# Kernel optimization log

Measured on AMD Instinct MI355X. Metric: run time of the kernel, lower is better.

## Reference

```python
import jax, jax.numpy as jnp
import numpy as np

N_NODES = 200000
N_EDGES = 600000
NUM_GRAPHS = 20000
IN_DIM = 128
HID = 128
HEADS1 = 4
OUT1 = HID // HEADS1  # 32
NEG_SLOPE = 0.2
LN_EPS = 1e-5


def setup_inputs() -> dict:
    key = jax.random.key(0)
    ks = jax.random.split(key, 12)
    x = jax.random.normal(ks[0], (N_NODES, IN_DIM), dtype=jnp.float32)
    edge_index = jax.random.randint(ks[1], (2, N_EDGES), 0, N_NODES, dtype=jnp.int64)
    batch = jnp.sort(jax.random.randint(ks[2], (N_NODES,), 0, NUM_GRAPHS, dtype=jnp.int64))
    s1 = 1.0 / np.sqrt(IN_DIM)
    s2 = 1.0 / np.sqrt(HID)
    W1 = jax.random.normal(ks[3], (IN_DIM, HEADS1 * OUT1), dtype=jnp.float32) * s1
    att_src1 = jax.random.normal(ks[4], (HEADS1, OUT1), dtype=jnp.float32) * s1
    att_dst1 = jax.random.normal(ks[5], (HEADS1, OUT1), dtype=jnp.float32) * s1
    b1 = jnp.zeros((HEADS1 * OUT1,), dtype=jnp.float32)
    W2 = jax.random.normal(ks[6], (HID, HID), dtype=jnp.float32) * s2
    att_src2 = jax.random.normal(ks[7], (1, HID), dtype=jnp.float32) * s2
    att_dst2 = jax.random.normal(ks[8], (1, HID), dtype=jnp.float32) * s2
    b2 = jnp.zeros((HID,), dtype=jnp.float32)
    ln_gamma = jnp.ones((HID,), dtype=jnp.float32)
    ln_beta = jnp.zeros((HID,), dtype=jnp.float32)
    return dict(x=x, edge_index=edge_index, batch=batch,
                W1=W1, att_src1=att_src1, att_dst1=att_dst1, b1=b1,
                W2=W2, att_src2=att_src2, att_dst2=att_dst2, b2=b2,
                ln_gamma=ln_gamma, ln_beta=ln_beta)


def gat_conv(x, W, att_src, att_dst, bias, edge_index, heads, out_ch):
    # PyG GATConv (concat=True, add_self_loops=True, eval mode / no dropout)
    n = x.shape[0]
    loop = jnp.arange(n, dtype=edge_index.dtype)
    src = jnp.concatenate([edge_index[0], loop])
    dst = jnp.concatenate([edge_index[1], loop])
    h = (x @ W).reshape(n, heads, out_ch)          # [N,H,C]
    a_src = jnp.einsum('nhc,hc->nh', h, att_src)    # [N,H]
    a_dst = jnp.einsum('nhc,hc->nh', h, att_dst)
    alpha = a_src[src] + a_dst[dst]                 # [E,H]
    alpha = jax.nn.leaky_relu(alpha, NEG_SLOPE)
    # segment softmax over incoming edges of each dst node
    m = jax.lax.stop_gradient(jax.ops.segment_max(alpha, dst, num_segments=n))
    e = jnp.exp(alpha - m[dst])
    denom = jax.ops.segment_sum(e, dst, num_segments=n)
    coef = e / denom[dst]                           # [E,H]
    msg = h[src] * coef[:, :, None]                 # [E,H,C]
    out = jax.ops.segment_sum(msg, dst, num_segments=n)  # [N,H,C]
    return out.reshape(n, heads * out_ch) + bias


def layer_norm(x, gamma, beta):
    mu = jnp.mean(x, axis=-1, keepdims=True)
    var = jnp.mean(jnp.square(x - mu), axis=-1, keepdims=True)
    return (x - mu) * jax.lax.rsqrt(var + LN_EPS) * gamma + beta


def reference(x, edge_index, batch, W1, att_src1, att_dst1, b1,
              W2, att_src2, att_dst2, b2, ln_gamma, ln_beta):
    h1 = jax.nn.relu(gat_conv(x, W1, att_src1, att_dst1, b1, edge_index, HEADS1, OUT1))
    h2 = gat_conv(h1, W2, att_src2, att_dst2, b2, edge_index, 1, HID)
    h2 = layer_norm(h2, ln_gamma, ln_beta)
    # global mean pool per graph
    sums = jax.ops.segment_sum(h2, batch, num_segments=NUM_GRAPHS)   # [G,HID]
    cnts = jax.ops.segment_sum(jnp.ones((h2.shape[0],), h2.dtype), batch, num_segments=NUM_GRAPHS)
    return sums / jnp.maximum(cnts, 1.0)[:, None]
```

## Files before the change

### kernel.cpp

```cpp
#include <hip/hip_runtime.h>
#include <cstdint>
#include <cstddef>

#define N_NODES_C 200000
#define N_EDGES_C 600000
#define NUM_GRAPHS_C 20000

constexpr float NEG_SLOPE = 0.2f;
constexpr float LN_EPS = 1e-5f;

typedef __attribute__((ext_vector_type(8))) short bf16x8;
typedef __attribute__((ext_vector_type(4))) float f32x4;

static __device__ __forceinline__ unsigned short f2bf(float f) {
  unsigned u = __float_as_uint(f);
  u = (u + 0x7fffu + ((u >> 16) & 1u)) >> 16;
  return (unsigned short)u;
}
static __device__ __forceinline__ float bf2f(unsigned short s) {
  return __uint_as_float(((unsigned)s) << 16);
}


__global__ __launch_bounds__(256) void count_deg_kernel(const int* __restrict__ dst,
                                                        int* __restrict__ deg, int E) {
  int e = blockIdx.x * 256 + threadIdx.x;
  if (e < E) atomicAdd(&deg[dst[e]], 1);
}

__global__ __launch_bounds__(256) void scan_kernel(const int* __restrict__ in,
                                                   int* __restrict__ out,
                                                   int* __restrict__ bsums, int n) {
  __shared__ int ss[256];
  int t = threadIdx.x;
  int base = blockIdx.x * 1024 + t * 4;
  int v[4];
  int s = 0;
#pragma unroll
  for (int j = 0; j < 4; ++j) {
    v[j] = (base + j < n) ? in[base + j] : 0;
    s += v[j];
  }
  ss[t] = s;
  __syncthreads();
  for (int off = 1; off < 256; off <<= 1) {
    int x = (t >= off) ? ss[t - off] : 0;
    __syncthreads();
    ss[t] += x;
    __syncthreads();
  }
  int incl = ss[t];
  int excl = incl - s;
  if (bsums != nullptr && t == 255) bsums[blockIdx.x] = incl;
  int run = excl;
#pragma unroll
  for (int j = 0; j < 4; ++j) {
    if (base + j < n) out[base + j] = run;
    run += v[j];
  }
}

__global__ __launch_bounds__(256) void scan_addoff_kernel(int* __restrict__ data,
                                                          const int* __restrict__ boff,
                                                          int n, int total) {
  int base = blockIdx.x * 1024 + threadIdx.x * 4;
  int add = boff[blockIdx.x];
#pragma unroll
  for (int j = 0; j < 4; ++j) {
    if (base + j < n) data[base + j] += add;
  }
  if (blockIdx.x == 0 && threadIdx.x == 0) data[n] = total;
}

__global__ __launch_bounds__(256) void fill_csr_kernel(const int* __restrict__ src,
                                                       const int* __restrict__ dst,
                                                       const int* __restrict__ row_ptr,
                                                       int* __restrict__ cursor,
                                                       int* __restrict__ col, int E) {
  int e = blockIdx.x * 256 + threadIdx.x;
  if (e < E) {
    int d = dst[e];
    int p = atomicAdd(&cursor[d], 1);
    col[row_ptr[d] + p] = src[e];
  }
}


__global__ __launch_bounds__(256) void graph_ptr_kernel(const int* __restrict__ batch,
                                                        int* __restrict__ gp, int n,
                                                        int G) {
  int i = blockIdx.x * 256 + threadIdx.x;
  if (i < n) {
    int prev = (i == 0) ? -1 : batch[i - 1];
    int cur = batch[i];
#pragma unroll 1
    for (int g = prev + 1; g <= cur; ++g) gp[g] = i;
  } else if (i == n) {
    int last = batch[n - 1];
#pragma unroll 1
    for (int g = last + 1; g <= G; ++g) gp[g] = n;
  }
}


__global__ __launch_bounds__(256) void wprep_kernel(const float* __restrict__ W,
                                                    unsigned short* __restrict__ Wtp) {
  int idx = blockIdx.x * 256 + threadIdx.x;
  if (idx >= 128 * 136) return;
  int n = idx / 136, k = idx % 136;
  Wtp[idx] = (k < 128) ? f2bf(W[(size_t)k * 128 + n]) : (unsigned short)0;
}


template <int H, bool A_BF16>
__global__ __launch_bounds__(256) void gemm_att_mfma(
    const void* __restrict__ Av, const unsigned short* __restrict__ Wtp,
    const float* __restrict__ att_src, const float* __restrict__ att_dst,
    unsigned short* __restrict__ Cbf, float* __restrict__ asrc,
    float* __restrict__ adst) {
  __shared__ __align__(16) unsigned short Alds[64 * 136];
  __shared__ __align__(16) unsigned short Wlds[128 * 136];
  int tid = threadIdx.x;
  int lane = tid & 63;
  int wave = tid >> 6;
  int row0 = blockIdx.x * 64;

#pragma unroll
  for (int i = 0; i < 9; ++i) {
    int ch = tid + i * 256;
    if (ch < 2176) *(bf16x8*)&Wlds[ch * 8] = *(const bf16x8*)&Wtp[(size_t)ch * 8];
  }
#pragma unroll
  for (int i = 0; i < 4; ++i) {
    int ch = tid + i * 256;
    int r = ch >> 4, c = ch & 15;
    if constexpr (A_BF16) {
      bf16x8 v = *(const bf16x8*)((const unsigned short*)Av +
                                  (size_t)(row0 + r) * 128 + c * 8);
      *(bf16x8*)&Alds[r * 136 + c * 8] = v;
    } else {
      const float* A = (const float*)Av;
      float4 v0 = *(const float4*)(A + (size_t)(row0 + r) * 128 + c * 8);
      float4 v1 = *(const float4*)(A + (size_t)(row0 + r) * 128 + c * 8 + 4);
      unsigned short tmp[8] = {f2bf(v0.x), f2bf(v0.y), f2bf(v0.z), f2bf(v0.w),
                               f2bf(v1.x), f2bf(v1.y), f2bf(v1.z), f2bf(v1.w)};
      *(bf16x8*)&Alds[r * 136 + c * 8] = *(bf16x8*)tmp;
    }
  }
  __syncthreads();

  int l15 = lane & 15;
  int lg = lane >> 4;
  int wr = wave * 16;

  f32x4 acc[8];
#pragma unroll
  for (int nt = 0; nt < 8; ++nt) acc[nt] = (f32x4){0.f, 0.f, 0.f, 0.f};

#pragma unroll
  for (int ks = 0; ks < 4; ++ks) {
    bf16x8 af = *(const bf16x8*)&Alds[(wr + l15) * 136 + ks * 32 + lg * 8];
#pragma unroll
    for (int nt = 0; nt < 8; ++nt) {
      bf16x8 bfr = *(const bf16x8*)&Wlds[(nt * 16 + l15) * 136 + ks * 32 + lg * 8];
      acc[nt] = __builtin_amdgcn_mfma_f32_16x16x32_bf16(af, bfr, acc[nt], 0, 0, 0);
    }
  }

  float vsv[8], vdv[8];
#pragma unroll
  for (int nt = 0; nt < 8; ++nt) {
    vsv[nt] = att_src[nt * 16 + l15];
    vdv[nt] = att_dst[nt * 16 + l15];
  }

#pragma unroll
  for (int r = 0; r < 4; ++r) {
    int row = row0 + wr + lg * 4 + r;
#pragma unroll
    for (int nt = 0; nt < 8; ++nt) {
      Cbf[(size_t)row * 128 + nt * 16 + l15] = f2bf(acc[nt][r]);
    }
    if constexpr (H == 4) {
      float ps[4], pd[4];
#pragma unroll
      for (int hd = 0; hd < 4; ++hd) {
        ps[hd] = acc[2 * hd][r] * vsv[2 * hd] + acc[2 * hd + 1][r] * vsv[2 * hd + 1];
        pd[hd] = acc[2 * hd][r] * vdv[2 * hd] + acc[2 * hd + 1][r] * vdv[2 * hd + 1];
#pragma unroll
        for (int off = 1; off < 16; off <<= 1) {
          ps[hd] += __shfl_xor(ps[hd], off, 64);
          pd[hd] += __shfl_xor(pd[hd], off, 64);
        }
      }
      if (l15 < 4) {
        float pss = (l15 == 0) ? ps[0] : (l15 == 1) ? ps[1] : (l15 == 2) ? ps[2] : ps[3];
        float pds = (l15 == 0) ? pd[0] : (l15 == 1) ? pd[1] : (l15 == 2) ? pd[2] : pd[3];
        asrc[(size_t)row * 4 + l15] = pss;
        adst[(size_t)row * 4 + l15] = pds;
      }
    } else {
      float ps = 0.f, pd = 0.f;
#pragma unroll
      for (int nt = 0; nt < 8; ++nt) {
        ps = fmaf(acc[nt][r], vsv[nt], ps);
        pd = fmaf(acc[nt][r], vdv[nt], pd);
      }
#pragma unroll
      for (int off = 1; off < 16; off <<= 1) {
        ps += __shfl_xor(ps, off, 64);
        pd += __shfl_xor(pd, off, 64);
      }
      if (l15 == 0) {
        asrc[row] = ps;
        adst[row] = pd;
      }
    }
  }
}


template <int H, bool RELU, bool LNOUT>
__global__ __launch_bounds__(256) void gat_agg3_kernel(
    const unsigned short* __restrict__ h, const float* __restrict__ asrc,
    const float* __restrict__ adst, const int* __restrict__ row_ptr,
    const int* __restrict__ col, const float* __restrict__ bias,
    const float* __restrict__ gamma, const float* __restrict__ beta,
    unsigned short* __restrict__ outbf, int n) {
  int wid = (blockIdx.x * 256 + threadIdx.x) >> 6;
  int lane = threadIdx.x & 63;
  int nodeA = wid * 2;
  int nodeB = nodeA + 1;
  if (nodeA >= n) return;
  bool hasB = nodeB < n;

  int e0A = row_ptr[nodeA];
  int e1A = row_ptr[nodeA + 1];
  int e1B = hasB ? row_ptr[nodeB + 1] : e1A;
  int e0B = e1A;
  int nedA = e1A - e0A;
  int nedB = e1B - e0B;

  int c0 = lane * 2;
  const int hd = (H == 1) ? 0 : (lane >> 4);

  float adA = (H == 4) ? adst[(size_t)nodeA * 4 + hd] : adst[nodeA];
  float asA = (H == 4) ? asrc[(size_t)nodeA * 4 + hd] : asrc[nodeA];
  int nB = hasB ? nodeB : nodeA;
  float adB = (H == 4) ? adst[(size_t)nB * 4 + hd] : adst[nB];
  float asB = (H == 4) ? asrc[(size_t)nB * 4 + hd] : asrc[nB];

  float xA = asA + adA; xA = (xA > 0.f) ? xA : NEG_SLOPE * xA;
  float selfeA = __expf(xA);
  float xB = asB + adB; xB = (xB > 0.f) ? xB : NEG_SLOPE * xB;
  float selfeB = __expf(xB);

  float denA = selfeA;
  float denB = selfeB;

  float2 accA, accB;
  {
    unsigned ha = *(const unsigned*)(h + (size_t)nodeA * 128 + c0);
    unsigned hb = *(const unsigned*)(h + (size_t)nB * 128 + c0);
    accA.x = bf2f((unsigned short)(ha & 0xffffu)) * selfeA;
    accA.y = bf2f((unsigned short)(ha >> 16)) * selfeA;
    accB.x = bf2f((unsigned short)(hb & 0xffffu)) * selfeB;
    accB.y = bf2f((unsigned short)(hb >> 16)) * selfeB;
  }

  int tmax = (nedA > nedB) ? nedA : nedB;
#pragma unroll 1
  for (int t = 0; t < tmax; t += 4) {
    int sA4[4], sB4[4];
    bool vA4[4], vB4[4];
#pragma unroll
    for (int i = 0; i < 4; ++i) {
      int e = t + i;
      vA4[i] = e < nedA;
      vB4[i] = hasB && e < nedB;
      sA4[i] = vA4[i] ? col[e0A + e] : nodeA;
      sB4[i] = vB4[i] ? col[e0B + e] : nodeA;
    }
    float aA4[4], aB4[4];
    unsigned hA4[4], hB4[4];
#pragma unroll
    for (int i = 0; i < 4; ++i) {
      aA4[i] = (H == 4) ? asrc[(size_t)sA4[i] * 4 + hd] : asrc[sA4[i]];
      aB4[i] = (H == 4) ? asrc[(size_t)sB4[i] * 4 + hd] : asrc[sB4[i]];
      hA4[i] = *(const unsigned*)(h + (size_t)sA4[i] * 128 + c0);
      hB4[i] = *(const unsigned*)(h + (size_t)sB4[i] * 128 + c0);
    }
#pragma unroll
    for (int i = 0; i < 4; ++i) {
      float ya = aA4[i] + adA; ya = (ya > 0.f) ? ya : NEG_SLOPE * ya;
      float eeA = vA4[i] ? __expf(ya) : 0.f;
      float yb = aB4[i] + adB; yb = (yb > 0.f) ? yb : NEG_SLOPE * yb;
      float eeB = vB4[i] ? __expf(yb) : 0.f;
      denA += eeA;
      denB += eeB;
      accA.x = fmaf(bf2f((unsigned short)(hA4[i] & 0xffffu)), eeA, accA.x);
      accA.y = fmaf(bf2f((unsigned short)(hA4[i] >> 16)), eeA, accA.y);
      accB.x = fmaf(bf2f((unsigned short)(hB4[i] & 0xffffu)), eeB, accB.x);
      accB.y = fmaf(bf2f((unsigned short)(hB4[i] >> 16)), eeB, accB.y);
    }
  }

  float invA = 1.f / denA;
  float invB = 1.f / denB;

  float bx = bias[c0], by = bias[c0 + 1];
  accA.x = fmaf(accA.x, invA, bx);
  accA.y = fmaf(accA.y, invA, by);
  accB.x = fmaf(accB.x, invB, bx);
  accB.y = fmaf(accB.y, invB, by);
  if (RELU) {
    accA.x = fmaxf(accA.x, 0.f); accA.y = fmaxf(accA.y, 0.f);
    accB.x = fmaxf(accB.x, 0.f); accB.y = fmaxf(accB.y, 0.f);
  }

  if (!LNOUT) {
    unsigned pa = (unsigned)f2bf(accA.x) | ((unsigned)f2bf(accA.y) << 16);
    *(unsigned*)(outbf + (size_t)nodeA * 128 + c0) = pa;
    if (hasB) {
      unsigned pb = (unsigned)f2bf(accB.x) | ((unsigned)f2bf(accB.y) << 16);
      *(unsigned*)(outbf + (size_t)nodeB * 128 + c0) = pb;
    }
  } else {
    float sA = accA.x + accA.y;
    float sB = accB.x + accB.y;
#pragma unroll
    for (int off = 1; off < 64; off <<= 1) {
      sA += __shfl_xor(sA, off, 64);
      sB += __shfl_xor(sB, off, 64);
    }
    float muA = sA * (1.f / 128.f), muB = sB * (1.f / 128.f);
    float dxA = accA.x - muA, dyA = accA.y - muA;
    float dxB = accB.x - muB, dyB = accB.y - muB;
    float vA = dxA * dxA + dyA * dyA;
    float vB = dxB * dxB + dyB * dyB;
#pragma unroll
    for (int off = 1; off < 64; off <<= 1) {
      vA += __shfl_xor(vA, off, 64);
      vB += __shfl_xor(vB, off, 64);
    }
    float ivA = rsqrtf(vA * (1.f / 128.f) + LN_EPS);
    float ivB = rsqrtf(vB * (1.f / 128.f) + LN_EPS);
    float gx = gamma[c0], gy = gamma[c0 + 1];
    float ex = beta[c0], ey = beta[c0 + 1];
    float oxA = fmaf(dxA * ivA, gx, ex), oyA = fmaf(dyA * ivA, gy, ey);
    unsigned pa = (unsigned)f2bf(oxA) | ((unsigned)f2bf(oyA) << 16);
    *(unsigned*)(outbf + (size_t)nodeA * 128 + c0) = pa;
    if (hasB) {
      float oxB = fmaf(dxB * ivB, gx, ex), oyB = fmaf(dyB * ivB, gy, ey);
      unsigned pb = (unsigned)f2bf(oxB) | ((unsigned)f2bf(oyB) << 16);
      *(unsigned*)(outbf + (size_t)nodeB * 128 + c0) = pb;
    }
  }
}


__global__ __launch_bounds__(256) void pool_kernel(const unsigned short* __restrict__ hln,
                                                   const int* __restrict__ gp,
                                                   float* __restrict__ out, int G) {
  int g = (blockIdx.x * 256 + threadIdx.x) >> 6;
  int lane = threadIdx.x & 63;
  if (g >= G) return;
  int s = gp[g], e = gp[g + 1];
  float ax = 0.f, ay = 0.f;
#pragma unroll 1
  for (int i = s; i < e; ++i) {
    unsigned v = *(const unsigned*)(hln + (size_t)i * 128 + lane * 2);
    ax += bf2f((unsigned short)(v & 0xffffu));
    ay += bf2f((unsigned short)(v >> 16));
  }
  int c = e - s;
  float sc = 1.f / (float)((c > 0) ? c : 1);
  *(float2*)(out + (size_t)g * 128 + lane * 2) = make_float2(ax * sc, ay * sc);
}


extern "C" void kernel_launch(void* const* d_in, const int* in_sizes, int n_in,
                              void* d_out, int out_size, void* d_ws, size_t ws_size,
                              hipStream_t stream) {
  const float* x = (const float*)d_in[0];
  const int* ei = (const int*)d_in[1];
  const int* batch = (const int*)d_in[2];
  const float* W1 = (const float*)d_in[3];
  const float* att_src1 = (const float*)d_in[4];
  const float* att_dst1 = (const float*)d_in[5];
  const float* b1 = (const float*)d_in[6];
  const float* W2 = (const float*)d_in[7];
  const float* att_src2 = (const float*)d_in[8];
  const float* att_dst2 = (const float*)d_in[9];
  const float* b2 = (const float*)d_in[10];
  const float* gamma = (const float*)d_in[11];
  const float* beta = (const float*)d_in[12];
  float* out = (float*)d_out;

  const int N = N_NODES_C, E = N_EDGES_C, G = NUM_GRAPHS_C;
  const int* src = ei;
  const int* dst = ei + E;

  float* p = (float*)d_ws;
  float* asrc1 = p; p += (size_t)N * 4;
  float* adst1 = p; p += (size_t)N * 4;
  float* asrc2 = p; p += N;
  float* adst2 = p; p += N;
  int* ip = (int*)p;
  int* deg = ip;       ip += N;
  int* cursor = ip;    ip += N;
  int* col = ip;       ip += E;
  int* bsums = ip;     ip += 256;
  int* bsums2 = ip;    ip += 256;
  int* row_ptr = ip;   ip += N + 2;
  int* graph_ptr = ip; ip += G + 2;
  unsigned short* h1bf = (unsigned short*)ip;
  unsigned short* hbbf = h1bf + (size_t)N * 128;
  unsigned short* h2bf = hbbf + (size_t)N * 128;
  unsigned short* wt1 = h2bf + (size_t)N * 128;
  unsigned short* wt2 = wt1 + 128 * 136;
  (void)ws_size; (void)in_sizes; (void)n_in; (void)out_size;

  hipMemsetAsync(deg, 0, sizeof(int) * (size_t)N, stream);
  hipMemsetAsync(cursor, 0, sizeof(int) * (size_t)N, stream);

  count_deg_kernel<<<(E + 255) / 256, 256, 0, stream>>>(dst, deg, E);
  int nblk = (N + 1023) / 1024;
  scan_kernel<<<nblk, 256, 0, stream>>>(deg, row_ptr, bsums, N);
  scan_kernel<<<1, 256, 0, stream>>>(bsums, bsums2, nullptr, nblk);
  scan_addoff_kernel<<<nblk, 256, 0, stream>>>(row_ptr, bsums2, N, E);
  fill_csr_kernel<<<(E + 255) / 256, 256, 0, stream>>>(src, dst, row_ptr, cursor, col, E);
  graph_ptr_kernel<<<(N + 1 + 255) / 256, 256, 0, stream>>>(batch, graph_ptr, N, G);
  wprep_kernel<<<(128 * 136 + 255) / 256, 256, 0, stream>>>(W1, wt1);
  wprep_kernel<<<(128 * 136 + 255) / 256, 256, 0, stream>>>(W2, wt2);

  int pairs = (N + 1) / 2;
  int pblocks = (int)(((size_t)pairs * 64 + 255) / 256);
  int gblocks = N / 64;

  gemm_att_mfma<4, false><<<gblocks, 256, 0, stream>>>(
      x, wt1, att_src1, att_dst1, h1bf, asrc1, adst1);
  gat_agg3_kernel<4, true, false><<<pblocks, 256, 0, stream>>>(
      h1bf, asrc1, adst1, row_ptr, col, b1, nullptr, nullptr, hbbf, N);

  gemm_att_mfma<1, true><<<gblocks, 256, 0, stream>>>(
      hbbf, wt2, att_src2, att_dst2, h2bf, asrc2, adst2);
  gat_agg3_kernel<1, false, true><<<pblocks, 256, 0, stream>>>(
      h2bf, asrc2, adst2, row_ptr, col, b2, gamma, beta, h1bf, N);

  pool_kernel<<<(int)(((size_t)G * 64 + 255) / 256), 256, 0, stream>>>(
      h1bf, graph_ptr, out, G);
}
```

Baseline: 297.3 us.

## Precompute per-edge attention exponentials in CSR order before aggregation

Adds an edge_score kernel that computes leaky-ReLU and exp of the attention logits per edge and scatters them into a head-major array indexed by CSR slot, recorded during CSR fill. The aggregation kernels then read these precomputed weights contiguously instead of gathering asrc for each source and evaluating exp per lane. The intent is to take the dependent random asrc gather off the aggregation critical path. The cost is two extra kernel launches, an extra edge-slot array, a scattered write pass, and reads of the column and weight arrays past the row end (masked, but EP padding is only 8).

Result: slower. 343.2 us (+15.4%).

```diff
diff --git a/kernel.cpp b/kernel.cpp
--- a/kernel.cpp
+++ b/kernel.cpp
@@ -76,12 +76,15 @@
                                                        const int* __restrict__ dst,
                                                        const int* __restrict__ row_ptr,
                                                        int* __restrict__ cursor,
-                                                       int* __restrict__ col, int E) {
+                                                       int* __restrict__ col,
+                                                       int* __restrict__ eslot, int E) {
   int e = blockIdx.x * 256 + threadIdx.x;
   if (e < E) {
     int d = dst[e];
     int p = atomicAdd(&cursor[d], 1);
-    col[row_ptr[d] + p] = src[e];
+    int slot = row_ptr[d] + p;
+    col[slot] = src[e];
+    eslot[e] = slot;
   }
 }
 
@@ -220,13 +223,39 @@
 }
 
 
+template <int H>
+__global__ __launch_bounds__(256) void edge_score_kernel(
+    const int* __restrict__ src, const int* __restrict__ dst,
+    const int* __restrict__ eslot, const float* __restrict__ asrc,
+    const float* __restrict__ adst, float* __restrict__ evt, int E, int EP) {
+  int e = blockIdx.x * 256 + threadIdx.x;
+  if (e >= E) return;
+  int s = src[e], d = dst[e], slot = eslot[e];
+  if constexpr (H == 4) {
+    float4 a = *(const float4*)(asrc + (size_t)s * 4);
+    float4 b = *(const float4*)(adst + (size_t)d * 4);
+    float v[4] = {a.x + b.x, a.y + b.y, a.z + b.z, a.w + b.w};
+#pragma unroll
+    for (int k = 0; k < 4; ++k) {
+      float x = v[k];
+      x = (x > 0.f) ? x : NEG_SLOPE * x;
+      evt[(size_t)k * EP + slot] = __expf(x);
+    }
+  } else {
+    float x = asrc[s] + adst[d];
+    x = (x > 0.f) ? x : NEG_SLOPE * x;
+    evt[slot] = __expf(x);
+  }
+}
+
+
 template <int H, bool RELU, bool LNOUT>
-__global__ __launch_bounds__(256) void gat_agg3_kernel(
+__global__ __launch_bounds__(256) void gat_agg4_kernel(
     const unsigned short* __restrict__ h, const float* __restrict__ asrc,
-    const float* __restrict__ adst, const int* __restrict__ row_ptr,
-    const int* __restrict__ col, const float* __restrict__ bias,
-    const float* __restrict__ gamma, const float* __restrict__ beta,
-    unsigned short* __restrict__ outbf, int n) {
+    const float* __restrict__ adst, const float* __restrict__ evt, int EP,
+    const int* __restrict__ row_ptr, const int* __restrict__ col,
+    const float* __restrict__ bias, const float* __restrict__ gamma,
+    const float* __restrict__ beta, unsigned short* __restrict__ outbf, int n) {
   int wid = (blockIdx.x * 256 + threadIdx.x) >> 6;
   int lane = threadIdx.x & 63;
   int nodeA = wid * 2;
@@ -243,6 +272,7 @@
 
   int c0 = lane * 2;
   const int hd = (H == 1) ? 0 : (lane >> 4);
+  const float* evh = evt + (size_t)hd * EP;
 
   float adA = (H == 4) ? adst[(size_t)nodeA * 4 + hd] : adst[nodeA];
   float asA = (H == 4) ? asrc[(size_t)nodeA * 4 + hd] : asrc[nodeA];
@@ -272,36 +302,35 @@
 #pragma unroll 1
   for (int t = 0; t < tmax; t += 4) {
     int sA4[4], sB4[4];
-    bool vA4[4], vB4[4];
+    float eA4[4], eB4[4];
 #pragma unroll
     for (int i = 0; i < 4; ++i) {
       int e = t + i;
-      vA4[i] = e < nedA;
-      vB4[i] = hasB && e < nedB;
-      sA4[i] = vA4[i] ? col[e0A + e] : nodeA;
-      sB4[i] = vB4[i] ? col[e0B + e] : nodeA;
-    }
-    float aA4[4], aB4[4];
+      bool vA = e < nedA;
+      bool vB = hasB && e < nedB;
+      int cA = col[e0A + e];
+      int cB = col[e0B + e];
+      float fA = evh[e0A + e];
+      float fB = evh[e0B + e];
+      sA4[i] = vA ? cA : nodeA;
+      sB4[i] = vB ? cB : nodeA;
+      eA4[i] = vA ? fA : 0.f;
+      eB4[i] = vB ? fB : 0.f;
+    }
     unsigned hA4[4], hB4[4];
 #pragma unroll
     for (int i = 0; i < 4; ++i) {
-      aA4[i] = (H == 4) ? asrc[(size_t)sA4[i] * 4 + hd] : asrc[sA4[i]];
-      aB4[i] = (H == 4) ? asrc[(size_t)sB4[i] * 4 + hd] : asrc[sB4[i]];
       hA4[i] = *(const unsigned*)(h + (size_t)sA4[i] * 128 + c0);
       hB4[i] = *(const unsigned*)(h + (size_t)sB4[i] * 128 + c0);
     }
 #pragma unroll
     for (int i = 0; i < 4; ++i) {
-      float ya = aA4[i] + adA; ya = (ya > 0.f) ? ya : NEG_SLOPE * ya;
-      float eeA = vA4[i] ? __expf(ya) : 0.f;
-      float yb = aB4[i] + adB; yb = (yb > 0.f) ? yb : NEG_SLOPE * yb;
-      float eeB = vB4[i] ? __expf(yb) : 0.f;
-      denA += eeA;
-      denB += eeB;
-      accA.x = fmaf(bf2f((unsigned short)(hA4[i] & 0xffffu)), eeA, accA.x);
-      accA.y = fmaf(bf2f((unsigned short)(hA4[i] >> 16)), eeA, accA.y);
-      accB.x = fmaf(bf2f((unsigned short)(hB4[i] & 0xffffu)), eeB, accB.x);
-      accB.y = fmaf(bf2f((unsigned short)(hB4[i] >> 16)), eeB, accB.y);
+      denA += eA4[i];
+      denB += eB4[i];
+      accA.x = fmaf(bf2f((unsigned short)(hA4[i] & 0xffffu)), eA4[i], accA.x);
+      accA.y = fmaf(bf2f((unsigned short)(hA4[i] >> 16)), eA4[i], accA.y);
+      accB.x = fmaf(bf2f((unsigned short)(hB4[i] & 0xffffu)), eB4[i], accB.x);
+      accB.y = fmaf(bf2f((unsigned short)(hB4[i] >> 16)), eB4[i], accB.y);
     }
   }
 
@@ -398,6 +427,7 @@
   float* out = (float*)d_out;
 
   const int N = N_NODES_C, E = N_EDGES_C, G = NUM_GRAPHS_C;
+  const int EP = E + 8;
   const int* src = ei;
   const int* dst = ei + E;
 
@@ -406,10 +436,13 @@
   float* adst1 = p; p += (size_t)N * 4;
   float* asrc2 = p; p += N;
   float* adst2 = p; p += N;
+  float* evt1 = p;  p += (size_t)EP * 4;
+  float* evt2 = p;  p += EP;
   int* ip = (int*)p;
   int* deg = ip;       ip += N;
   int* cursor = ip;    ip += N;
   int* col = ip;       ip += E;
+  int* eslot = ip;     ip += E;
   int* bsums = ip;     ip += 256;
   int* bsums2 = ip;    ip += 256;
   int* row_ptr = ip;   ip += N + 2;
@@ -429,24 +462,30 @@
   scan_kernel<<<nblk, 256, 0, stream>>>(deg, row_ptr, bsums, N);
   scan_kernel<<<1, 256, 0, stream>>>(bsums, bsums2, nullptr, nblk);
   scan_addoff_kernel<<<nblk, 256, 0, stream>>>(row_ptr, bsums2, N, E);
-  fill_csr_kernel<<<(E + 255) / 256, 256, 0, stream>>>(src, dst, row_ptr, cursor, col, E);
+  fill_csr_kernel<<<(E + 255) / 256, 256, 0, stream>>>(src, dst, row_ptr, cursor, col,
+                                                       eslot, E);
   graph_ptr_kernel<<<(N + 1 + 255) / 256, 256, 0, stream>>>(batch, graph_ptr, N, G);
   wprep_kernel<<<(128 * 136 + 255) / 256, 256, 0, stream>>>(W1, wt1);
   wprep_kernel<<<(128 * 136 + 255) / 256, 256, 0, stream>>>(W2, wt2);
 
   int pairs = (N + 1) / 2;
   int pblocks = (int)(((size_t)pairs * 64 + 255) / 256);
+  int eblocks = (E + 255) / 256;
   int gblocks = N / 64;
 
   gemm_att_mfma<4, false><<<gblocks, 256, 0, stream>>>(
       x, wt1, att_src1, att_dst1, h1bf, asrc1, adst1);
-  gat_agg3_kernel<4, true, false><<<pblocks, 256, 0, stream>>>(
-      h1bf, asrc1, adst1, row_ptr, col, b1, nullptr, nullptr, hbbf, N);
+  edge_score_kernel<4><<<eblocks, 256, 0, stream>>>(src, dst, eslot, asrc1, adst1,
+                                                    evt1, E, EP);
+  gat_agg4_kernel<4, true, false><<<pblocks, 256, 0, stream>>>(
+      h1bf, asrc1, adst1, evt1, EP, row_ptr, col, b1, nullptr, nullptr, hbbf, N);
 
   gemm_att_mfma<1, true><<<gblocks, 256, 0, stream>>>(
       hbbf, wt2, att_src2, att_dst2, h2bf, asrc2, adst2);
-  gat_agg3_kernel<1, false, true><<<pblocks, 256, 0, stream>>>(
-      h2bf, asrc2, adst2, row_ptr, col, b2, gamma, beta, h1bf, N);
+  edge_score_kernel<1><<<eblocks, 256, 0, stream>>>(src, dst, eslot, asrc2, adst2,
+                                                    evt2, E, EP);
+  gat_agg4_kernel<1, false, true><<<pblocks, 256, 0, stream>>>(
+      h2bf, asrc2, adst2, evt2, EP, row_ptr, col, b2, gamma, beta, h1bf, N);
 
   pool_kernel<<<(int)(((size_t)G * 64 + 255) / 256), 256, 0, stream>>>(
       h1bf, graph_ptr, out, G);
```

## Pad CSR rows to multiples of four with dummy node to drop bounds checks

Applied to the files above, without the earlier changes.

Each CSR row is padded to a multiple of four plus at least four extra slots, filled with a dummy source node N whose attention score is set to -1e30 so its exp weight is zero. The aggregation loop then loads col entries without per-edge validity predicates and keeps indices wave-uniform via readfirstlane, so neighbor indices sit in scalar registers. The cost is a larger col array, an extra pad-fill kernel and a tiny init kernel, plus wasted gathers of the dummy row for padded slots. The dummy node's h row is never written, so correctness relies on exp(-1e30) being exactly zero even if that row holds stale data. The odd-node tail handling is removed, which works because N is even.

Result: slower. 322.2 us (+8.4%).

```diff
diff --git a/kernel.cpp b/kernel.cpp
--- a/kernel.cpp
+++ b/kernel.cpp
@@ -30,7 +30,8 @@
 
 __global__ __launch_bounds__(256) void scan_kernel(const int* __restrict__ in,
                                                    int* __restrict__ out,
-                                                   int* __restrict__ bsums, int n) {
+                                                   int* __restrict__ bsums,
+                                                   int n_total, int npad) {
   __shared__ int ss[256];
   int t = threadIdx.x;
   int base = blockIdx.x * 1024 + t * 4;
@@ -38,8 +39,11 @@
   int s = 0;
 #pragma unroll
   for (int j = 0; j < 4; ++j) {
-    v[j] = (base + j < n) ? in[base + j] : 0;
-    s += v[j];
+    int idx = base + j;
+    int x = (idx < n_total) ? in[idx] : 0;
+    if (idx < npad) x = ((x + 3) & ~3) + 4;
+    v[j] = x;
+    s += x;
   }
   ss[t] = s;
   __syncthreads();
@@ -55,21 +59,20 @@
   int run = excl;
 #pragma unroll
   for (int j = 0; j < 4; ++j) {
-    if (base + j < n) out[base + j] = run;
+    if (base + j < n_total) out[base + j] = run;
     run += v[j];
   }
 }
 
 __global__ __launch_bounds__(256) void scan_addoff_kernel(int* __restrict__ data,
                                                           const int* __restrict__ boff,
-                                                          int n, int total) {
+                                                          int n_total) {
   int base = blockIdx.x * 1024 + threadIdx.x * 4;
   int add = boff[blockIdx.x];
 #pragma unroll
   for (int j = 0; j < 4; ++j) {
-    if (base + j < n) data[base + j] += add;
-  }
-  if (blockIdx.x == 0 && threadIdx.x == 0) data[n] = total;
+    if (base + j < n_total) data[base + j] += add;
+  }
 }
 
 __global__ __launch_bounds__(256) void fill_csr_kernel(const int* __restrict__ src,
@@ -83,6 +86,24 @@
     int p = atomicAdd(&cursor[d], 1);
     col[row_ptr[d] + p] = src[e];
   }
+}
+
+__global__ __launch_bounds__(256) void pad_fill_kernel(const int* __restrict__ row_ptr,
+                                                       const int* __restrict__ deg,
+                                                       int* __restrict__ col, int n) {
+  int i = blockIdx.x * 256 + threadIdx.x;
+  if (i >= n) return;
+  int s = row_ptr[i] + deg[i];
+  int e = row_ptr[i + 1];
+#pragma unroll 1
+  for (int j = s; j < e; ++j) col[j] = n;
+}
+
+__global__ void dummy_init_kernel(float* __restrict__ asrc1,
+                                  float* __restrict__ asrc2, int n) {
+  int t = threadIdx.x;
+  if (t < 4) asrc1[(size_t)n * 4 + t] = -1e30f;
+  if (t == 4) asrc2[n] = -1e30f;
 }
 
 
@@ -221,34 +242,32 @@
 
 
 template <int H, bool RELU, bool LNOUT>
-__global__ __launch_bounds__(256) void gat_agg3_kernel(
+__global__ __launch_bounds__(256) void gat_agg5_kernel(
     const unsigned short* __restrict__ h, const float* __restrict__ asrc,
     const float* __restrict__ adst, const int* __restrict__ row_ptr,
     const int* __restrict__ col, const float* __restrict__ bias,
     const float* __restrict__ gamma, const float* __restrict__ beta,
     unsigned short* __restrict__ outbf, int n) {
-  int wid = (blockIdx.x * 256 + threadIdx.x) >> 6;
+  int wid = __builtin_amdgcn_readfirstlane((blockIdx.x * 256 + threadIdx.x) >> 6);
   int lane = threadIdx.x & 63;
   int nodeA = wid * 2;
   int nodeB = nodeA + 1;
   if (nodeA >= n) return;
-  bool hasB = nodeB < n;
-
-  int e0A = row_ptr[nodeA];
-  int e1A = row_ptr[nodeA + 1];
-  int e1B = hasB ? row_ptr[nodeB + 1] : e1A;
-  int e0B = e1A;
-  int nedA = e1A - e0A;
-  int nedB = e1B - e0B;
+
+  int e0A = __builtin_amdgcn_readfirstlane(row_ptr[nodeA]);
+  int e0B = __builtin_amdgcn_readfirstlane(row_ptr[nodeA + 1]);
+  int e1B = __builtin_amdgcn_readfirstlane(row_ptr[nodeA + 2]);
+  int lastA = e0B - e0A - 4;
+  int lastB = e1B - e0B - 4;
+  int tmax = ((lastA > lastB) ? lastA : lastB) + 4;
 
   int c0 = lane * 2;
   const int hd = (H == 1) ? 0 : (lane >> 4);
 
   float adA = (H == 4) ? adst[(size_t)nodeA * 4 + hd] : adst[nodeA];
   float asA = (H == 4) ? asrc[(size_t)nodeA * 4 + hd] : asrc[nodeA];
-  int nB = hasB ? nodeB : nodeA;
-  float adB = (H == 4) ? adst[(size_t)nB * 4 + hd] : adst[nB];
-  float asB = (H == 4) ? asrc[(size_t)nB * 4 + hd] : asrc[nB];
+  float adB = (H == 4) ? adst[(size_t)nodeB * 4 + hd] : adst[nodeB];
+  float asB = (H == 4) ? asrc[(size_t)nodeB * 4 + hd] : asrc[nodeB];
 
   float xA = asA + adA; xA = (xA > 0.f) ? xA : NEG_SLOPE * xA;
   float selfeA = __expf(xA);
@@ -261,25 +280,22 @@
   float2 accA, accB;
   {
     unsigned ha = *(const unsigned*)(h + (size_t)nodeA * 128 + c0);
-    unsigned hb = *(const unsigned*)(h + (size_t)nB * 128 + c0);
+    unsigned hb = *(const unsigned*)(h + (size_t)nodeB * 128 + c0);
     accA.x = bf2f((unsigned short)(ha & 0xffffu)) * selfeA;
     accA.y = bf2f((unsigned short)(ha >> 16)) * selfeA;
     accB.x = bf2f((unsigned short)(hb & 0xffffu)) * selfeB;
     accB.y = bf2f((unsigned short)(hb >> 16)) * selfeB;
   }
 
-  int tmax = (nedA > nedB) ? nedA : nedB;
 #pragma unroll 1
   for (int t = 0; t < tmax; t += 4) {
+    int tA = (t < lastA) ? t : lastA;
+    int tB = (t < lastB) ? t : lastB;
     int sA4[4], sB4[4];
-    bool vA4[4], vB4[4];
 #pragma unroll
     for (int i = 0; i < 4; ++i) {
-      int e = t + i;
-      vA4[i] = e < nedA;
-      vB4[i] = hasB && e < nedB;
-      sA4[i] = vA4[i] ? col[e0A + e] : nodeA;
-      sB4[i] = vB4[i] ? col[e0B + e] : nodeA;
+      sA4[i] = __builtin_amdgcn_readfirstlane(col[e0A + tA + i]);
+      sB4[i] = __builtin_amdgcn_readfirstlane(col[e0B + tB + i]);
     }
     float aA4[4], aB4[4];
     unsigned hA4[4], hB4[4];
@@ -293,9 +309,9 @@
 #pragma unroll
     for (int i = 0; i < 4; ++i) {
       float ya = aA4[i] + adA; ya = (ya > 0.f) ? ya : NEG_SLOPE * ya;
-      float eeA = vA4[i] ? __expf(ya) : 0.f;
+      float eeA = __expf(ya);
       float yb = aB4[i] + adB; yb = (yb > 0.f) ? yb : NEG_SLOPE * yb;
-      float eeB = vB4[i] ? __expf(yb) : 0.f;
+      float eeB = __expf(yb);
       denA += eeA;
       denB += eeB;
       accA.x = fmaf(bf2f((unsigned short)(hA4[i] & 0xffffu)), eeA, accA.x);
@@ -320,11 +336,9 @@
 
   if (!LNOUT) {
     unsigned pa = (unsigned)f2bf(accA.x) | ((unsigned)f2bf(accA.y) << 16);
+    unsigned pb = (unsigned)f2bf(accB.x) | ((unsigned)f2bf(accB.y) << 16);
     *(unsigned*)(outbf + (size_t)nodeA * 128 + c0) = pa;
-    if (hasB) {
-      unsigned pb = (unsigned)f2bf(accB.x) | ((unsigned)f2bf(accB.y) << 16);
-      *(unsigned*)(outbf + (size_t)nodeB * 128 + c0) = pb;
-    }
+    *(unsigned*)(outbf + (size_t)nodeB * 128 + c0) = pb;
   } else {
     float sA = accA.x + accA.y;
     float sB = accB.x + accB.y;
@@ -348,13 +362,11 @@
     float gx = gamma[c0], gy = gamma[c0 + 1];
     float ex = beta[c0], ey = beta[c0 + 1];
     float oxA = fmaf(dxA * ivA, gx, ex), oyA = fmaf(dyA * ivA, gy, ey);
+    float oxB = fmaf(dxB * ivB, gx, ex), oyB = fmaf(dyB * ivB, gy, ey);
     unsigned pa = (unsigned)f2bf(oxA) | ((unsigned)f2bf(oyA) << 16);
+    unsigned pb = (unsigned)f2bf(oxB) | ((unsigned)f2bf(oyB) << 16);
     *(unsigned*)(outbf + (size_t)nodeA * 128 + c0) = pa;
-    if (hasB) {
-      float oxB = fmaf(dxB * ivB, gx, ex), oyB = fmaf(dyB * ivB, gy, ey);
-      unsigned pb = (unsigned)f2bf(oxB) | ((unsigned)f2bf(oyB) << 16);
-      *(unsigned*)(outbf + (size_t)nodeB * 128 + c0) = pb;
-    }
+    *(unsigned*)(outbf + (size_t)nodeB * 128 + c0) = pb;
   }
 }
 
@@ -398,54 +410,57 @@
   float* out = (float*)d_out;
 
   const int N = N_NODES_C, E = N_EDGES_C, G = NUM_GRAPHS_C;
+  const int COLSZ = E + 7 * N;
   const int* src = ei;
   const int* dst = ei + E;
 
   float* p = (float*)d_ws;
-  float* asrc1 = p; p += (size_t)N * 4;
+  float* asrc1 = p; p += (size_t)(N + 1) * 4;
   float* adst1 = p; p += (size_t)N * 4;
-  float* asrc2 = p; p += N;
+  float* asrc2 = p; p += N + 1;
   float* adst2 = p; p += N;
   int* ip = (int*)p;
-  int* deg = ip;       ip += N;
+  int* deg = ip;       ip += N + 1;
   int* cursor = ip;    ip += N;
-  int* col = ip;       ip += E;
+  int* col = ip;       ip += COLSZ;
   int* bsums = ip;     ip += 256;
   int* bsums2 = ip;    ip += 256;
   int* row_ptr = ip;   ip += N + 2;
   int* graph_ptr = ip; ip += G + 2;
   unsigned short* h1bf = (unsigned short*)ip;
-  unsigned short* hbbf = h1bf + (size_t)N * 128;
-  unsigned short* h2bf = hbbf + (size_t)N * 128;
-  unsigned short* wt1 = h2bf + (size_t)N * 128;
+  unsigned short* hbbf = h1bf + (size_t)(N + 1) * 128;
+  unsigned short* h2bf = hbbf + (size_t)(N + 1) * 128;
+  unsigned short* wt1 = h2bf + (size_t)(N + 1) * 128;
   unsigned short* wt2 = wt1 + 128 * 136;
   (void)ws_size; (void)in_sizes; (void)n_in; (void)out_size;
 
-  hipMemsetAsync(deg, 0, sizeof(int) * (size_t)N, stream);
+  hipMemsetAsync(deg, 0, sizeof(int) * (size_t)(N + 1), stream);
   hipMemsetAsync(cursor, 0, sizeof(int) * (size_t)N, stream);
 
   count_deg_kernel<<<(E + 255) / 256, 256, 0, stream>>>(dst, deg, E);
-  int nblk = (N + 1023) / 1024;
-  scan_kernel<<<nblk, 256, 0, stream>>>(deg, row_ptr, bsums, N);
-  scan_kernel<<<1, 256, 0, stream>>>(bsums, bsums2, nullptr, nblk);
-  scan_addoff_kernel<<<nblk, 256, 0, stream>>>(row_ptr, bsums2, N, E);
+  int nblk = (N + 1 + 1023) / 1024;
+  scan_kernel<<<nblk, 256, 0, stream>>>(deg, row_ptr, bsums, N + 1, N);
+  scan_kernel<<<1, 256, 0, stream>>>(bsums, bsums2, nullptr, nblk, 0);
+  scan_addoff_kernel<<<nblk, 256, 0, stream>>>(row_ptr, bsums2, N + 1);
   fill_csr_kernel<<<(E + 255) / 256, 256, 0, stream>>>(src, dst, row_ptr, cursor, col, E);
+  pad_fill_kernel<<<(N + 255) / 256, 256, 0, stream>>>(row_ptr, deg, col, N);
   graph_ptr_kernel<<<(N + 1 + 255) / 256, 256, 0, stream>>>(batch, graph_ptr, N, G);
   wprep_kernel<<<(128 * 136 + 255) / 256, 256, 0, stream>>>(W1, wt1);
   wprep_kernel<<<(128 * 136 + 255) / 256, 256, 0, stream>>>(W2, wt2);
-
-  int pairs = (N + 1) / 2;
+  dummy_init_kernel<<<1, 64, 0, stream>>>(asrc1, asrc2, N);
+
+  int pairs = N / 2;
   int pblocks = (int)(((size_t)pairs * 64 + 255) / 256);
   int gblocks = N / 64;
 
   gemm_att_mfma<4, false><<<gblocks, 256, 0, stream>>>(
       x, wt1, att_src1, att_dst1, h1bf, asrc1, adst1);
-  gat_agg3_kernel<4, true, false><<<pblocks, 256, 0, stream>>>(
+  gat_agg5_kernel<4, true, false><<<pblocks, 256, 0, stream>>>(
       h1bf, asrc1, adst1, row_ptr, col, b1, nullptr, nullptr, hbbf, N);
 
   gemm_att_mfma<1, true><<<gblocks, 256, 0, stream>>>(
       hbbf, wt2, att_src2, att_dst2, h2bf, asrc2, adst2);
-  gat_agg3_kernel<1, false, true><<<pblocks, 256, 0, stream>>>(
+  gat_agg5_kernel<1, false, true><<<pblocks, 256, 0, stream>>>(
       h2bf, asrc2, adst2, row_ptr, col, b2, gamma, beta, h1bf, N);
 
   pool_kernel<<<(int)(((size_t)G * 64 + 255) / 256), 256, 0, stream>>>(
```
